# Kernel tuning notes

Hardware: AMD Instinct MI355X
Metric: run time of the kernel (lower is better)

## Reference

```python
import jax, jax.numpy as jnp
import numpy as np

N_FFT = 1024
HOP = 256


def _hann_periodic(n):
    # torch.hann_window default (periodic=True): 0.5*(1 - cos(2*pi*k/n))
    k = jnp.arange(n, dtype=jnp.float32)
    return 0.5 * (1.0 - jnp.cos(2.0 * jnp.pi * k / n))


def setup_inputs() -> dict:
    key = jax.random.key(0)
    x = jax.random.normal(key, (32, 2, 513, 1024, 2), dtype=jnp.float32)
    return {"x": x}


def reference(x):
    B, C, F, T, _ = x.shape
    n_fft = 2 * (F - 1)          # 1024
    hop = HOP
    # complex spectrum, frames along last-but-one axis -> (B*C, T, F)
    spec = jax.lax.complex(x[..., 0], x[..., 1])
    spec = spec.reshape(B * C, F, T).transpose(0, 2, 1)
    # torch.irfft(normalized=True) = true inverse * sqrt(n_fft)
    frames = jnp.fft.irfft(spec, n=n_fft, axis=-1) * np.float32(np.sqrt(n_fft))
    frames = frames * _hann_periodic(n_fft)[None, None, :]  # (BC, T, n_fft)
    # vectorized overlap-add (scatter-add)
    L = n_fft + hop * (T - 1)
    idx = jnp.arange(T)[:, None] * hop + jnp.arange(n_fft)[None, :]  # (T, n_fft)
    y = jnp.zeros((B * C, L), dtype=x.dtype).at[:, idx].add(frames)
    y = y[:, n_fft // 2:]
    coeff = n_fft / float(hop) / 2.0
    return (y / coeff).reshape(B, C, -1)
```

## Files before the change

kernel.cpp:

```cpp
#include <hip/hip_runtime.h>
#include <math.h>

#define NFFT 1024
#define HOP 256
#define NFREQ 513
#define TFRAMES 1024
#define NT_TILE 8
#define LOUT  262400
#define NPAIR 1408

__device__ __forceinline__ float2 cadd(float2 a, float2 b){ return make_float2(a.x+b.x, a.y+b.y); }
__device__ __forceinline__ float2 csub(float2 a, float2 b){ return make_float2(a.x-b.x, a.y-b.y); }
__device__ __forceinline__ float2 muli(float2 a){ return make_float2(-a.y, a.x); }
__device__ __forceinline__ float2 cmul(float2 a, float2 b){
    return make_float2(a.x*b.x - a.y*b.y, a.x*b.y + a.y*b.x);
}

__device__ __forceinline__ void radix8_inv(float2& v0, float2& v1, float2& v2, float2& v3,
                                           float2& v4, float2& v5, float2& v6, float2& v7) {
    const float C = 0.70710678118654752f;
    float2 a0 = cadd(v0, v4), a1 = csub(v0, v4);
    float2 a2 = cadd(v2, v6), a3 = csub(v2, v6);
    float2 b0 = cadd(v1, v5), b1 = csub(v1, v5);
    float2 b2 = cadd(v3, v7), b3 = csub(v3, v7);
    float2 E0 = cadd(a0, a2), E2 = csub(a0, a2);
    float2 E1 = cadd(a1, muli(a3)), E3 = csub(a1, muli(a3));
    float2 O0 = cadd(b0, b2), O2 = csub(b0, b2);
    float2 O1 = cadd(b1, muli(b3)), O3 = csub(b1, muli(b3));
    float2 T1 = make_float2(C*(O1.x - O1.y),  C*(O1.x + O1.y));
    float2 T2 = muli(O2);
    float2 T3 = make_float2(-C*(O3.x + O3.y), C*(O3.x - O3.y));
    v0 = cadd(E0, O0); v4 = csub(E0, O0);
    v1 = cadd(E1, T1); v5 = csub(E1, T1);
    v2 = cadd(E2, T2); v6 = csub(E2, T2);
    v3 = cadd(E3, T3); v7 = csub(E3, T3);
}

__device__ __forceinline__ int zpos(int n) {
    int blk = n >> 6;
    return blk * 64 + ((n & 63) ^ ((9 * blk) & 63));
}

__global__ __launch_bounds__(512, 4) void istft_kernel(const float2* __restrict__ x,
                                                       float* __restrict__ out) {
    __shared__ float2 Zc[8 * 512];

    const int tid  = threadIdx.x;
    const int bc   = blockIdx.y;
    const int tile = blockIdx.x;
    const int t0   = tile * NT_TILE;
    const int S0   = t0 * HOP;

    const float HR = 0.99998117528260111f, HI = 0.00613588464915448f;
    const float C8 = 0.92387953251128676f, S8 = 0.38268343236508977f;
    const float A512 = 0.012271846303085130f;

    {
        const int kg = tid >> 3, tt = tid & 7;
        const int tg = t0 + tt;
        const long baseIn = (long)bc * ((long)NFREQ * TFRAMES);
        const int wbase = tt << 9;
        const int fxw = tt << 1;
        float twr, twi;
        __sincosf((float)kg * 0.0061359231515425649f , &twi, &twr);
        twr *= 0.5f; twi *= 0.5f;
        #pragma unroll
        for (int i = 0; i < 5; ++i) {
            int kp = kg + 64 * i;
            if (kp <= 256) {
                float2 A = x[baseIn + (long)kp * TFRAMES + tg];
                float2 B = x[baseIn + (long)(512 - kp) * TFRAMES + tg];
                if (kp == 0) { A.y = 0.f; B.y = 0.f; }
                float d2r = A.x - B.x, d2i = A.y + B.y;
                float o2r = twr * d2r - twi * d2i, o2i = twr * d2i + twi * d2r;
                float s2r = 0.5f * (A.x + B.x), s2i = 0.5f * (A.y - B.y);
                Zc[wbase + (zpos(kp) ^ fxw)] = make_float2(s2r - o2i, s2i + o2r);
                if (kp >= 1 && kp <= 255)
                    Zc[wbase + (zpos(512 - kp) ^ fxw)] = make_float2(s2r + o2i, o2r - s2i);
            }
            float nr = twr * C8 - twi * S8;
            twi = twr * S8 + twi * C8; twr = nr;
        }
    }
    __syncthreads();

    const int f     = tid >> 6;
    const int lane6 = tid & 63;
    const int fbase = f << 9;
    const int fx    = f << 1;

    {
        const int j = lane6, jx = lane6 ^ fx, zb = fbase;
        float2 v0 = Zc[zb +       (jx ^  0)];
        float2 v1 = Zc[zb +  64 + (jx ^  9)];
        float2 v2 = Zc[zb + 128 + (jx ^ 18)];
        float2 v3 = Zc[zb + 192 + (jx ^ 27)];
        float2 v4 = Zc[zb + 256 + (jx ^ 36)];
        float2 v5 = Zc[zb + 320 + (jx ^ 45)];
        float2 v6 = Zc[zb + 384 + (jx ^ 54)];
        float2 v7 = Zc[zb + 448 + (jx ^ 63)];
        radix8_inv(v0, v1, v2, v3, v4, v5, v6, v7);
        float sw_, cw_;
        __sincosf((float)j * A512, &sw_, &cw_);
        float2 w1 = make_float2(cw_, sw_);
        float2 w2 = cmul(w1, w1);
        float2 w3 = cmul(w2, w1);
        float2 w4 = cmul(w2, w2);
        float2 w5 = cmul(w3, w2);
        float2 w6 = cmul(w3, w3);
        float2 w7 = cmul(w4, w3);
        Zc[zb +       (jx ^  0)] = v0;
        Zc[zb +  64 + (jx ^  9)] = cmul(v1, w1);
        Zc[zb + 128 + (jx ^ 18)] = cmul(v2, w2);
        Zc[zb + 192 + (jx ^ 27)] = cmul(v3, w3);
        Zc[zb + 256 + (jx ^ 36)] = cmul(v4, w4);
        Zc[zb + 320 + (jx ^ 45)] = cmul(v5, w5);
        Zc[zb + 384 + (jx ^ 54)] = cmul(v6, w6);
        Zc[zb + 448 + (jx ^ 63)] = cmul(v7, w7);
    }
    {
        const int b = lane6 >> 3, jp = lane6 & 7;
        const int sw = ((9 * b) & 63) ^ fx, bb = fbase + 64 * b;
        float2 v0 = Zc[bb + ((jp     ) ^ sw)];
        float2 v1 = Zc[bb + ((jp +  8) ^ sw)];
        float2 v2 = Zc[bb + ((jp + 16) ^ sw)];
        float2 v3 = Zc[bb + ((jp + 24) ^ sw)];
        float2 v4 = Zc[bb + ((jp + 32) ^ sw)];
        float2 v5 = Zc[bb + ((jp + 40) ^ sw)];
        float2 v6 = Zc[bb + ((jp + 48) ^ sw)];
        float2 v7 = Zc[bb + ((jp + 56) ^ sw)];
        radix8_inv(v0, v1, v2, v3, v4, v5, v6, v7);
        float sw_, cw_;
        __sincosf((float)jp * 0.098174770424681039f , &sw_, &cw_);
        float2 w1 = make_float2(cw_, sw_);
        float2 w2 = cmul(w1, w1);
        float2 w3 = cmul(w2, w1);
        float2 w4 = cmul(w2, w2);
        float2 w5 = cmul(w3, w2);
        float2 w6 = cmul(w3, w3);
        float2 w7 = cmul(w4, w3);
        Zc[bb + ((jp     ) ^ sw)] = v0;
        Zc[bb + ((jp +  8) ^ sw)] = cmul(v1, w1);
        Zc[bb + ((jp + 16) ^ sw)] = cmul(v2, w2);
        Zc[bb + ((jp + 24) ^ sw)] = cmul(v3, w3);
        Zc[bb + ((jp + 32) ^ sw)] = cmul(v4, w4);
        Zc[bb + ((jp + 40) ^ sw)] = cmul(v5, w5);
        Zc[bb + ((jp + 48) ^ sw)] = cmul(v6, w6);
        Zc[bb + ((jp + 56) ^ sw)] = cmul(v7, w7);
    }
    {
        const int b = lane6 >> 3, g = lane6 & 7;
        const int sw = ((9 * b) & 63) ^ fx, bb = fbase + 64 * b, g8 = 8 * g;
        float2 v0 = Zc[bb + ((g8    ) ^ sw)];
        float2 v1 = Zc[bb + ((g8 + 1) ^ sw)];
        float2 v2 = Zc[bb + ((g8 + 2) ^ sw)];
        float2 v3 = Zc[bb + ((g8 + 3) ^ sw)];
        float2 v4 = Zc[bb + ((g8 + 4) ^ sw)];
        float2 v5 = Zc[bb + ((g8 + 5) ^ sw)];
        float2 v6 = Zc[bb + ((g8 + 6) ^ sw)];
        float2 v7 = Zc[bb + ((g8 + 7) ^ sw)];
        radix8_inv(v0, v1, v2, v3, v4, v5, v6, v7);
        Zc[bb + ((g8    ) ^ sw)] = v0;
        Zc[bb + ((g8 + 1) ^ sw)] = v1;
        Zc[bb + ((g8 + 2) ^ sw)] = v2;
        Zc[bb + ((g8 + 3) ^ sw)] = v3;
        Zc[bb + ((g8 + 4) ^ sw)] = v4;
        Zc[bb + ((g8 + 5) ^ sw)] = v5;
        Zc[bb + ((g8 + 6) ^ sw)] = v6;
        Zc[bb + ((g8 + 7) ^ sw)] = v7;
    }
    __syncthreads();


    {
        const int pi = tid;
        const int slh = pi >> 7;
        const int k0 = pi & 7;
        const int hi = ((pi >> 3) & 7) << 3;
        const int k2v = pi >> 6;
        const int sw9 = (9 * k0) & 63;
        float se, ce;
        __sincosf((float)pi * A512, &se, &ce);
        float ae = 0.f, ao = 0.f;
        const int cb = k0 << 6;
        #pragma unroll 4
        for (int u = 0; u <= slh; ++u) {
            int low = ((hi | (k2v - 2 * u)) ^ sw9) ^ (u << 1);
            float2 zz = Zc[cb + (u << 9) + low];
            float cou = ce * HR - se * HI;
            ae += zz.x * (1.f - ce);
            ao += zz.y * (1.f - cou);
            float nc = se; se = -ce; ce = nc;
        }
        ae *= 0.015625f; ao *= 0.015625f;
        int s = S0 + (pi << 1);
        int o = bc * LOUT + (s - 512);
        if (pi >= 384) {
            reinterpret_cast<float2*>(out)[o >> 1] = make_float2(ae, ao);
        } else if (s >= 512) {
            atomicAdd(&out[o],     ae);
            atomicAdd(&out[o + 1], ao);
        }
    }

    {
        const int pi = tid + 512;
        const int slh = pi >> 7;
        const int tlo = slh - 3;
        const int m0 = pi - (tlo << 7);
        const int k0 = m0 & 7;
        const int hi = ((m0 >> 3) & 7) << 3;
        const int k2v = m0 >> 6;
        const int sw9 = (9 * k0) & 63;
        float se0, ce0;
        __sincosf((float)m0 * A512, &se0, &ce0);
        const float ce = ce0, se = se0;
        const int cb = (tlo << 9) + (k0 << 6);

        {
            float ae = 0.f, ao = 0.f;
            #pragma unroll
            for (int u = 0; u < 4; ++u) {
                int low = ((hi | (k2v - 2 * u)) ^ sw9) ^ ((tlo + u) << 1);
                float2 zz = Zc[cb + (u << 9) + low];
                float cu = (u == 0) ? ce : (u == 1) ? se : (u == 2) ? -ce : -se;
                float su = (u == 0) ? se : (u == 1) ? -ce : (u == 2) ? -se : ce;
                float cou = cu * HR - su * HI;
                ae += zz.x * (1.f - cu);
                ao += zz.y * (1.f - cou);
            }
            ae *= 0.015625f; ao *= 0.015625f;
            int s = S0 + (pi << 1);
            reinterpret_cast<float2*>(out)[(bc * LOUT + (s - 512)) >> 1] = make_float2(ae, ao);
        }

        if (tid < 384) {
            const int ntap = 4 - tlo;
            float ce2 = ce, se2 = se;
            float ae = 0.f, ao = 0.f;
            const int cb2 = cb + (4 << 9);
            #pragma unroll 3
            for (int u = 0; u < ntap; ++u) {
                int low = ((hi | (k2v - 2 * u)) ^ sw9) ^ ((tlo + 4 + u) << 1);
                float2 zz = Zc[cb2 + (u << 9) + low];
                float cou = ce2 * HR - se2 * HI;
                ae += zz.x * (1.f - ce2);
                ao += zz.y * (1.f - cou);
                float nc = se2; se2 = -ce2; ce2 = nc;
            }
            ae *= 0.015625f; ao *= 0.015625f;
            int s = S0 + ((pi + 512) << 1);
            int o = bc * LOUT + (s - 512);
            atomicAdd(&out[o],     ae);
            atomicAdd(&out[o + 1], ao);
        }
    }
}

extern "C" void kernel_launch(void* const* d_in, const int* in_sizes, int n_in,
                              void* d_out, int out_size, void* d_ws, size_t ws_size,
                              hipStream_t stream) {
    const float2* x = (const float2*)d_in[0];
    float* out = (float*)d_out;
    (void)in_sizes; (void)n_in; (void)d_ws; (void)ws_size;

    hipMemsetAsync(d_out, 0, (size_t)out_size * sizeof(float), stream);

    dim3 grid(TFRAMES / NT_TILE, 64);
    dim3 block(512);
    istft_kernel<<<grid, block, 0, stream>>>(x, out);
}
```

Before: 129.1 us.

## Recompute halo frames per tile to drop atomics and output memset

Each tile now also loads and inverse-FFTs the next three frames (a halo), so it can produce its whole output span by itself with plain vectorized float4 stores. This removes the atomicAdd overlap-add across tiles and the hipMemsetAsync of the output buffer. The cost is about 37% more FFT work and input reads per tile, plus more shared memory (11 frames), which may lower occupancy. The first tile handles its leading region separately.

```diff
diff --git a/kernel.cpp b/kernel.cpp
--- a/kernel.cpp
+++ b/kernel.cpp
@@ -7,7 +7,6 @@
 #define TFRAMES 1024
 #define NT_TILE 8
 #define LOUT  262400
-#define NPAIR 1408
 
 __device__ __forceinline__ float2 cadd(float2 a, float2 b){ return make_float2(a.x+b.x, a.y+b.y); }
 __device__ __forceinline__ float2 csub(float2 a, float2 b){ return make_float2(a.x-b.x, a.y-b.y); }
@@ -41,15 +40,99 @@
     return blk * 64 + ((n & 63) ^ ((9 * blk) & 63));
 }
 
+__device__ __forceinline__ void fft_frame(float2* Zc, int fr, int lane6) {
+    const float A512 = 0.012271846303085130f;
+    const int fx = fr << 1;
+    {
+        const int j = lane6, jx = lane6 ^ fx, zb = fr << 9;
+        float2 v0 = Zc[zb +       (jx ^  0)];
+        float2 v1 = Zc[zb +  64 + (jx ^  9)];
+        float2 v2 = Zc[zb + 128 + (jx ^ 18)];
+        float2 v3 = Zc[zb + 192 + (jx ^ 27)];
+        float2 v4 = Zc[zb + 256 + (jx ^ 36)];
+        float2 v5 = Zc[zb + 320 + (jx ^ 45)];
+        float2 v6 = Zc[zb + 384 + (jx ^ 54)];
+        float2 v7 = Zc[zb + 448 + (jx ^ 63)];
+        radix8_inv(v0, v1, v2, v3, v4, v5, v6, v7);
+        float swf, cwf;
+        __sincosf((float)j * A512, &swf, &cwf);
+        float2 w1 = make_float2(cwf, swf);
+        float2 w2 = cmul(w1, w1);
+        float2 w3 = cmul(w2, w1);
+        float2 w4 = cmul(w2, w2);
+        float2 w5 = cmul(w3, w2);
+        float2 w6 = cmul(w3, w3);
+        float2 w7 = cmul(w4, w3);
+        Zc[zb +       (jx ^  0)] = v0;
+        Zc[zb +  64 + (jx ^  9)] = cmul(v1, w1);
+        Zc[zb + 128 + (jx ^ 18)] = cmul(v2, w2);
+        Zc[zb + 192 + (jx ^ 27)] = cmul(v3, w3);
+        Zc[zb + 256 + (jx ^ 36)] = cmul(v4, w4);
+        Zc[zb + 320 + (jx ^ 45)] = cmul(v5, w5);
+        Zc[zb + 384 + (jx ^ 54)] = cmul(v6, w6);
+        Zc[zb + 448 + (jx ^ 63)] = cmul(v7, w7);
+    }
+    {
+        const int b = lane6 >> 3, jp = lane6 & 7;
+        const int sw = ((9 * b) & 63) ^ fx, bb = (fr << 9) + 64 * b;
+        float2 v0 = Zc[bb + ((jp     ) ^ sw)];
+        float2 v1 = Zc[bb + ((jp +  8) ^ sw)];
+        float2 v2 = Zc[bb + ((jp + 16) ^ sw)];
+        float2 v3 = Zc[bb + ((jp + 24) ^ sw)];
+        float2 v4 = Zc[bb + ((jp + 32) ^ sw)];
+        float2 v5 = Zc[bb + ((jp + 40) ^ sw)];
+        float2 v6 = Zc[bb + ((jp + 48) ^ sw)];
+        float2 v7 = Zc[bb + ((jp + 56) ^ sw)];
+        radix8_inv(v0, v1, v2, v3, v4, v5, v6, v7);
+        float swf, cwf;
+        __sincosf((float)jp * 0.098174770424681039f , &swf, &cwf);
+        float2 w1 = make_float2(cwf, swf);
+        float2 w2 = cmul(w1, w1);
+        float2 w3 = cmul(w2, w1);
+        float2 w4 = cmul(w2, w2);
+        float2 w5 = cmul(w3, w2);
+        float2 w6 = cmul(w3, w3);
+        float2 w7 = cmul(w4, w3);
+        Zc[bb + ((jp     ) ^ sw)] = v0;
+        Zc[bb + ((jp +  8) ^ sw)] = cmul(v1, w1);
+        Zc[bb + ((jp + 16) ^ sw)] = cmul(v2, w2);
+        Zc[bb + ((jp + 24) ^ sw)] = cmul(v3, w3);
+        Zc[bb + ((jp + 32) ^ sw)] = cmul(v4, w4);
+        Zc[bb + ((jp + 40) ^ sw)] = cmul(v5, w5);
+        Zc[bb + ((jp + 48) ^ sw)] = cmul(v6, w6);
+        Zc[bb + ((jp + 56) ^ sw)] = cmul(v7, w7);
+    }
+    {
+        const int b = lane6 >> 3, g = lane6 & 7;
+        const int sw = ((9 * b) & 63) ^ fx, bb = (fr << 9) + 64 * b, g8 = 8 * g;
+        float2 v0 = Zc[bb + ((g8    ) ^ sw)];
+        float2 v1 = Zc[bb + ((g8 + 1) ^ sw)];
+        float2 v2 = Zc[bb + ((g8 + 2) ^ sw)];
+        float2 v3 = Zc[bb + ((g8 + 3) ^ sw)];
+        float2 v4 = Zc[bb + ((g8 + 4) ^ sw)];
+        float2 v5 = Zc[bb + ((g8 + 5) ^ sw)];
+        float2 v6 = Zc[bb + ((g8 + 6) ^ sw)];
+        float2 v7 = Zc[bb + ((g8 + 7) ^ sw)];
+        radix8_inv(v0, v1, v2, v3, v4, v5, v6, v7);
+        Zc[bb + ((g8    ) ^ sw)] = v0;
+        Zc[bb + ((g8 + 1) ^ sw)] = v1;
+        Zc[bb + ((g8 + 2) ^ sw)] = v2;
+        Zc[bb + ((g8 + 3) ^ sw)] = v3;
+        Zc[bb + ((g8 + 4) ^ sw)] = v4;
+        Zc[bb + ((g8 + 5) ^ sw)] = v5;
+        Zc[bb + ((g8 + 6) ^ sw)] = v6;
+        Zc[bb + ((g8 + 7) ^ sw)] = v7;
+    }
+}
+
 __global__ __launch_bounds__(512, 4) void istft_kernel(const float2* __restrict__ x,
                                                        float* __restrict__ out) {
-    __shared__ float2 Zc[8 * 512];
+    __shared__ float2 Zc[11 * 512];
 
     const int tid  = threadIdx.x;
     const int bc   = blockIdx.y;
     const int tile = blockIdx.x;
     const int t0   = tile * NT_TILE;
-    const int S0   = t0 * HOP;
 
     const float HR = 0.99998117528260111f, HI = 0.00613588464915448f;
     const float C8 = 0.92387953251128676f, S8 = 0.38268343236508977f;
@@ -82,178 +165,119 @@
             twi = twr * S8 + twi * C8; twr = nr;
         }
     }
+    if (tile != 127) {
+        const int kg2 = tid >> 2, ft = tid & 3;
+        const int f2 = 8 + ft;
+        const int tg2 = t0 + f2;
+        const long baseIn = (long)bc * ((long)NFREQ * TFRAMES);
+        const int wb2 = f2 << 9;
+        const int fx2 = f2 << 1;
+        float t2r, t2i;
+        __sincosf((float)kg2 * 0.0061359231515425649f, &t2i, &t2r);
+        t2r *= 0.5f; t2i *= 0.5f;
+        const float C4 = 0.70710678118654752f;
+        #pragma unroll
+        for (int i = 0; i < 3; ++i) {
+            int kp = kg2 + 128 * i;
+            if (ft < 3 && kp <= 256) {
+                float2 A = x[baseIn + (long)kp * TFRAMES + tg2];
+                float2 B = x[baseIn + (long)(512 - kp) * TFRAMES + tg2];
+                if (kp == 0) { A.y = 0.f; B.y = 0.f; }
+                float d2r = A.x - B.x, d2i = A.y + B.y;
+                float o2r = t2r * d2r - t2i * d2i, o2i = t2r * d2i + t2i * d2r;
+                float s2r = 0.5f * (A.x + B.x), s2i = 0.5f * (A.y - B.y);
+                Zc[wb2 + (zpos(kp) ^ fx2)] = make_float2(s2r - o2i, s2i + o2r);
+                if (kp >= 1 && kp <= 255)
+                    Zc[wb2 + (zpos(512 - kp) ^ fx2)] = make_float2(s2r + o2i, o2r - s2i);
+            }
+            float nr = t2r * C4 - t2i * C4;
+            t2i = t2r * C4 + t2i * C4; t2r = nr;
+        }
+    }
     __syncthreads();
 
     const int f     = tid >> 6;
     const int lane6 = tid & 63;
-    const int fbase = f << 9;
-    const int fx    = f << 1;
-
-    {
-        const int j = lane6, jx = lane6 ^ fx, zb = fbase;
-        float2 v0 = Zc[zb +       (jx ^  0)];
-        float2 v1 = Zc[zb +  64 + (jx ^  9)];
-        float2 v2 = Zc[zb + 128 + (jx ^ 18)];
-        float2 v3 = Zc[zb + 192 + (jx ^ 27)];
-        float2 v4 = Zc[zb + 256 + (jx ^ 36)];
-        float2 v5 = Zc[zb + 320 + (jx ^ 45)];
-        float2 v6 = Zc[zb + 384 + (jx ^ 54)];
-        float2 v7 = Zc[zb + 448 + (jx ^ 63)];
-        radix8_inv(v0, v1, v2, v3, v4, v5, v6, v7);
-        float sw_, cw_;
-        __sincosf((float)j * A512, &sw_, &cw_);
-        float2 w1 = make_float2(cw_, sw_);
-        float2 w2 = cmul(w1, w1);
-        float2 w3 = cmul(w2, w1);
-        float2 w4 = cmul(w2, w2);
-        float2 w5 = cmul(w3, w2);
-        float2 w6 = cmul(w3, w3);
-        float2 w7 = cmul(w4, w3);
-        Zc[zb +       (jx ^  0)] = v0;
-        Zc[zb +  64 + (jx ^  9)] = cmul(v1, w1);
-        Zc[zb + 128 + (jx ^ 18)] = cmul(v2, w2);
-        Zc[zb + 192 + (jx ^ 27)] = cmul(v3, w3);
-        Zc[zb + 256 + (jx ^ 36)] = cmul(v4, w4);
-        Zc[zb + 320 + (jx ^ 45)] = cmul(v5, w5);
-        Zc[zb + 384 + (jx ^ 54)] = cmul(v6, w6);
-        Zc[zb + 448 + (jx ^ 63)] = cmul(v7, w7);
-    }
-    {
-        const int b = lane6 >> 3, jp = lane6 & 7;
-        const int sw = ((9 * b) & 63) ^ fx, bb = fbase + 64 * b;
-        float2 v0 = Zc[bb + ((jp     ) ^ sw)];
-        float2 v1 = Zc[bb + ((jp +  8) ^ sw)];
-        float2 v2 = Zc[bb + ((jp + 16) ^ sw)];
-        float2 v3 = Zc[bb + ((jp + 24) ^ sw)];
-        float2 v4 = Zc[bb + ((jp + 32) ^ sw)];
-        float2 v5 = Zc[bb + ((jp + 40) ^ sw)];
-        float2 v6 = Zc[bb + ((jp + 48) ^ sw)];
-        float2 v7 = Zc[bb + ((jp + 56) ^ sw)];
-        radix8_inv(v0, v1, v2, v3, v4, v5, v6, v7);
-        float sw_, cw_;
-        __sincosf((float)jp * 0.098174770424681039f , &sw_, &cw_);
-        float2 w1 = make_float2(cw_, sw_);
-        float2 w2 = cmul(w1, w1);
-        float2 w3 = cmul(w2, w1);
-        float2 w4 = cmul(w2, w2);
-        float2 w5 = cmul(w3, w2);
-        float2 w6 = cmul(w3, w3);
-        float2 w7 = cmul(w4, w3);
-        Zc[bb + ((jp     ) ^ sw)] = v0;
-        Zc[bb + ((jp +  8) ^ sw)] = cmul(v1, w1);
-        Zc[bb + ((jp + 16) ^ sw)] = cmul(v2, w2);
-        Zc[bb + ((jp + 24) ^ sw)] = cmul(v3, w3);
-        Zc[bb + ((jp + 32) ^ sw)] = cmul(v4, w4);
-        Zc[bb + ((jp + 40) ^ sw)] = cmul(v5, w5);
-        Zc[bb + ((jp + 48) ^ sw)] = cmul(v6, w6);
-        Zc[bb + ((jp + 56) ^ sw)] = cmul(v7, w7);
-    }
-    {
-        const int b = lane6 >> 3, g = lane6 & 7;
-        const int sw = ((9 * b) & 63) ^ fx, bb = fbase + 64 * b, g8 = 8 * g;
-        float2 v0 = Zc[bb + ((g8    ) ^ sw)];
-        float2 v1 = Zc[bb + ((g8 + 1) ^ sw)];
-        float2 v2 = Zc[bb + ((g8 + 2) ^ sw)];
-        float2 v3 = Zc[bb + ((g8 + 3) ^ sw)];
-        float2 v4 = Zc[bb + ((g8 + 4) ^ sw)];
-        float2 v5 = Zc[bb + ((g8 + 5) ^ sw)];
-        float2 v6 = Zc[bb + ((g8 + 6) ^ sw)];
-        float2 v7 = Zc[bb + ((g8 + 7) ^ sw)];
-        radix8_inv(v0, v1, v2, v3, v4, v5, v6, v7);
-        Zc[bb + ((g8    ) ^ sw)] = v0;
-        Zc[bb + ((g8 + 1) ^ sw)] = v1;
-        Zc[bb + ((g8 + 2) ^ sw)] = v2;
-        Zc[bb + ((g8 + 3) ^ sw)] = v3;
-        Zc[bb + ((g8 + 4) ^ sw)] = v4;
-        Zc[bb + ((g8 + 5) ^ sw)] = v5;
-        Zc[bb + ((g8 + 6) ^ sw)] = v6;
-        Zc[bb + ((g8 + 7) ^ sw)] = v7;
-    }
+
+    fft_frame(Zc, f, lane6);
+    if (tile != 127 && f < 3) fft_frame(Zc, 8 + f, lane6);
     __syncthreads();
 
-
-    {
-        const int pi = tid;
-        const int slh = pi >> 7;
-        const int k0 = pi & 7;
-        const int hi = ((pi >> 3) & 7) << 3;
-        const int k2v = pi >> 6;
-        const int sw9 = (9 * k0) & 63;
-        float se, ce;
-        __sincosf((float)pi * A512, &se, &ce);
-        float ae = 0.f, ao = 0.f;
-        const int cb = k0 << 6;
-        #pragma unroll 4
-        for (int u = 0; u <= slh; ++u) {
-            int low = ((hi | (k2v - 2 * u)) ^ sw9) ^ (u << 1);
-            float2 zz = Zc[cb + (u << 9) + low];
-            float cou = ce * HR - se * HI;
-            ae += zz.x * (1.f - ce);
-            ao += zz.y * (1.f - cou);
-            float nc = se; se = -ce; ce = nc;
-        }
-        ae *= 0.015625f; ao *= 0.015625f;
-        int s = S0 + (pi << 1);
-        int o = bc * LOUT + (s - 512);
-        if (pi >= 384) {
-            reinterpret_cast<float2*>(out)[o >> 1] = make_float2(ae, ao);
-        } else if (s >= 512) {
-            atomicAdd(&out[o],     ae);
-            atomicAdd(&out[o + 1], ao);
-        }
-    }
-
-    {
-        const int pi = tid + 512;
-        const int slh = pi >> 7;
+    {
+        const int pi0 = 384 + (tid << 1);
+        const int sl0 = pi0 << 1;
+        const int slh = sl0 >> 8;
         const int tlo = slh - 3;
-        const int m0 = pi - (tlo << 7);
-        const int k0 = m0 & 7;
-        const int hi = ((m0 >> 3) & 7) << 3;
+        const int m0  = 384 + (pi0 & 127);
+        const int k0  = m0 & 7;
+        const int hi  = ((m0 >> 3) & 7) << 3;
         const int k2v = m0 >> 6;
-        const int sw9 = (9 * k0) & 63;
-        float se0, ce0;
+        const int sw9  = (9 * k0) & 63;
+        const int sw9b = sw9 + 9;
+        float se0, ce0, se1, ce1;
         __sincosf((float)m0 * A512, &se0, &ce0);
-        const float ce = ce0, se = se0;
+        __sincosf((float)(m0 + 1) * A512, &se1, &ce1);
+        float ae0 = 0.f, ao0 = 0.f, ae1 = 0.f, ao1 = 0.f;
         const int cb = (tlo << 9) + (k0 << 6);
-
-        {
-            float ae = 0.f, ao = 0.f;
+        if (tile != 127) {
             #pragma unroll
             for (int u = 0; u < 4; ++u) {
-                int low = ((hi | (k2v - 2 * u)) ^ sw9) ^ ((tlo + u) << 1);
-                float2 zz = Zc[cb + (u << 9) + low];
-                float cu = (u == 0) ? ce : (u == 1) ? se : (u == 2) ? -ce : -se;
-                float su = (u == 0) ? se : (u == 1) ? -ce : (u == 2) ? -se : ce;
-                float cou = cu * HR - su * HI;
-                ae += zz.x * (1.f - cu);
-                ao += zz.y * (1.f - cou);
-            }
-            ae *= 0.015625f; ao *= 0.015625f;
-            int s = S0 + (pi << 1);
-            reinterpret_cast<float2*>(out)[(bc * LOUT + (s - 512)) >> 1] = make_float2(ae, ao);
-        }
-
-        if (tid < 384) {
-            const int ntap = 4 - tlo;
-            float ce2 = ce, se2 = se;
-            float ae = 0.f, ao = 0.f;
-            const int cb2 = cb + (4 << 9);
-            #pragma unroll 3
+                const int rx = (tlo + u) << 1;
+                const int hk = hi | (k2v - 2 * u);
+                float2 zA = Zc[cb +      (u << 9) + ((hk ^ sw9 ) ^ rx)];
+                float2 zB = Zc[cb + 64 + (u << 9) + ((hk ^ sw9b) ^ rx)];
+                float cA = (u == 0) ? ce0 : (u == 1) ? se0 : (u == 2) ? -ce0 : -se0;
+                float sA = (u == 0) ? se0 : (u == 1) ? -ce0 : (u == 2) ? -se0 : ce0;
+                float cB = (u == 0) ? ce1 : (u == 1) ? se1 : (u == 2) ? -ce1 : -se1;
+                float sB = (u == 0) ? se1 : (u == 1) ? -ce1 : (u == 2) ? -se1 : ce1;
+                ae0 += zA.x * (1.f - cA);
+                ao0 += zA.y * (1.f - (cA * HR - sA * HI));
+                ae1 += zB.x * (1.f - cB);
+                ao1 += zB.y * (1.f - (cB * HR - sB * HI));
+            }
+        } else {
+            const int ntap = (slh <= 7) ? 4 : (11 - slh);
+            float ceA = ce0, seA = se0, ceB = ce1, seB = se1;
+            #pragma unroll 4
             for (int u = 0; u < ntap; ++u) {
-                int low = ((hi | (k2v - 2 * u)) ^ sw9) ^ ((tlo + 4 + u) << 1);
-                float2 zz = Zc[cb2 + (u << 9) + low];
-                float cou = ce2 * HR - se2 * HI;
-                ae += zz.x * (1.f - ce2);
-                ao += zz.y * (1.f - cou);
-                float nc = se2; se2 = -ce2; ce2 = nc;
-            }
-            ae *= 0.015625f; ao *= 0.015625f;
-            int s = S0 + ((pi + 512) << 1);
-            int o = bc * LOUT + (s - 512);
-            atomicAdd(&out[o],     ae);
-            atomicAdd(&out[o + 1], ao);
-        }
+                const int rx = (tlo + u) << 1;
+                const int hk = hi | (k2v - 2 * u);
+                float2 zA = Zc[cb +      (u << 9) + ((hk ^ sw9 ) ^ rx)];
+                float2 zB = Zc[cb + 64 + (u << 9) + ((hk ^ sw9b) ^ rx)];
+                ae0 += zA.x * (1.f - ceA);
+                ao0 += zA.y * (1.f - (ceA * HR - seA * HI));
+                ae1 += zB.x * (1.f - ceB);
+                ao1 += zB.y * (1.f - (ceB * HR - seB * HI));
+                float nA = seA; seA = -ceA; ceA = nA;
+                float nB = seB; seB = -ceB; ceB = nB;
+            }
+        }
+        const int o = bc * LOUT + (tile << 11) + 256 + (tid << 2);
+        reinterpret_cast<float4*>(out)[o >> 2] =
+            make_float4(ae0 * 0.015625f, ao0 * 0.015625f, ae1 * 0.015625f, ao1 * 0.015625f);
+    }
+
+    if (tile == 0 && tid < 128) {
+        const int pi  = 256 + tid;
+        const int k0e = pi & 7;
+        const int hie = ((pi >> 3) & 7) << 3;
+        const int k2e = pi >> 6;
+        const int sw9e = (9 * k0e) & 63;
+        float see, cee;
+        __sincosf((float)pi * A512, &see, &cee);
+        float ae = 0.f, ao = 0.f;
+        const int cbe = k0e << 6;
+        #pragma unroll
+        for (int u = 0; u < 3; ++u) {
+            const int rx = u << 1;
+            const int hk = hie | (k2e - 2 * u);
+            float2 zz = Zc[cbe + (u << 9) + ((hk ^ sw9e) ^ rx)];
+            ae += zz.x * (1.f - cee);
+            ao += zz.y * (1.f - (cee * HR - see * HI));
+            float nc = see; see = -cee; cee = nc;
+        }
+        const int o = bc * LOUT + ((pi - 256) << 1);
+        reinterpret_cast<float2*>(out)[o >> 1] = make_float2(ae * 0.015625f, ao * 0.015625f);
     }
 }
 
@@ -262,9 +286,7 @@
                               hipStream_t stream) {
     const float2* x = (const float2*)d_in[0];
     float* out = (float*)d_out;
-    (void)in_sizes; (void)n_in; (void)d_ws; (void)ws_size;
-
-    hipMemsetAsync(d_out, 0, (size_t)out_size * sizeof(float), stream);
+    (void)in_sizes; (void)n_in; (void)d_ws; (void)ws_size; (void)out_size;
 
     dim3 grid(TFRAMES / NT_TILE, 64);
     dim3 block(512);
```

After: 155.0 us. 1.2x slower.
